# Kernel tuning notes

Measured on AMD Instinct MI355X. Metric: run time of the kernel, lower is better.

## Reference

```python
import jax, jax.numpy as jnp
import numpy as np

EPS = 1e-5  # torch BatchNorm2d default eps


def _lin(x, W, b):
    # torch nn.Linear: y = x @ W.T + b, W is [out, in]
    return jnp.einsum('...i,oi->...o', x, W) + b


def _bn(x, g, b):
    # BatchNorm2d in training mode: normalize per channel (last axis here)
    # over all other axes (B, N, K) with biased variance.
    m = jnp.mean(x, axis=(0, 1, 2), keepdims=True)
    v = jnp.mean(jnp.square(x - m), axis=(0, 1, 2), keepdims=True)
    return (x - m) * jax.lax.rsqrt(v + EPS) * g + b


def _gelu(x):
    return jax.nn.gelu(x, approximate=False)  # torch F.gelu default is erf


def _knn_idx(points, k):
    # squared euclidean pairwise distances, then k smallest per query
    pn = jnp.sum(points * points, axis=-1)  # [B,N]
    d2 = pn[:, :, None] + pn[:, None, :] - 2.0 * jnp.einsum('bnd,bmd->bnm', points, points)
    _, idx = jax.lax.top_k(-d2, k)  # [B,N,k], nearest first (includes self)
    return idx


def _gather(x, idx):
    # x: [B,N,D], idx: [B,N,K] -> [B,N,K,D]
    return jax.vmap(lambda a, i: a[i])(x, idx)


def setup_inputs() -> dict:
    key = jax.random.key(0)
    ks = jax.random.split(key, 20)
    B, N, Dp, Df, k = 2, 8192, 3, 128, 16

    def lin_params(kw, kb, din, dout):
        s = 1.0 / np.sqrt(din)
        W = jax.random.uniform(kw, (dout, din), jnp.float32, -s, s)
        b = jax.random.uniform(kb, (dout,), jnp.float32, -s, s)
        return W, b

    Wq, bq = lin_params(ks[0], ks[1], Df, Df)
    Wk, bk = lin_params(ks[2], ks[3], Df, Df)
    Wv, bv = lin_params(ks[4], ks[5], Df, Df)
    Wd1, bd1 = lin_params(ks[6], ks[7], Dp, Dp)
    Wd2, bd2 = lin_params(ks[8], ks[9], Dp, Df)
    Wg1, bg1 = lin_params(ks[10], ks[11], Df, Df)
    Wg2, bg2 = lin_params(ks[12], ks[13], Df, Df)

    return {
        'feats': jax.random.normal(ks[14], (B, N, Df), jnp.float32),
        'points': jax.random.normal(ks[15], (B, N, Dp), jnp.float32),
        'Wq': Wq, 'bq': bq, 'Wk': Wk, 'bk': bk, 'Wv': Wv, 'bv': bv,
        'Wd1': Wd1, 'bd1': bd1, 'Wd2': Wd2, 'bd2': bd2,
        'Wg1': Wg1, 'bg1': bg1, 'Wg2': Wg2, 'bg2': bg2,
        'gd': jnp.ones((Dp,), jnp.float32), 'betad': jnp.zeros((Dp,), jnp.float32),
        'gg1': jnp.ones((Df,), jnp.float32), 'betag1': jnp.zeros((Df,), jnp.float32),
        'gg2': jnp.ones((Df,), jnp.float32), 'betag2': jnp.zeros((Df,), jnp.float32),
        'k': 16,
    }


def reference(feats, points, Wq, bq, Wk, bk, Wv, bv, Wd1, bd1, Wd2, bd2,
              Wg1, bg1, Wg2, bg2, gd, betad, gg1, betag1, gg2, betag2, k):
    idx = _knn_idx(points, k)                     # [B,N,k]
    knn_feats = _gather(feats, idx)               # [B,N,k,Df]
    knn_points = _gather(points, idx)             # [B,N,k,Dp]

    pos = points[:, :, None, :] - knn_points      # [B,N,k,Dp]
    pos = _lin(pos, Wd1, bd1)
    pos = _gelu(_bn(pos, gd, betad))
    pos = _lin(pos, Wd2, bd2)                     # [B,N,k,Df]

    q = _lin(feats, Wq, bq)                       # [B,N,Df]
    key_t = _lin(knn_feats, Wk, bk)               # [B,N,k,Df]
    gamma = q[:, :, None, :] - key_t + pos
    gamma = _gelu(_bn(gamma, gg1, betag1))
    gamma = _lin(gamma, Wg1, bg1)
    gamma = _gelu(_bn(gamma, gg2, betag2))
    gamma = _lin(gamma, Wg2, bg2)

    rho = jax.nn.softmax(gamma, axis=-2)          # softmax over k neighbors
    value = _lin(knn_feats, Wv, bv) + pos
    return jnp.einsum('bnkd,bnkd->bnd', rho, value)
```

## Files before the change

kernel.cpp:

```cpp
#include <hip/hip_runtime.h>
#include <hip/hip_bf16.h>
#include <math.h>

#define NPTS 8192
#define STAT_CNT 262144.0f
#define BN_EPS 1e-5f

typedef __attribute__((__ext_vector_type__(8))) __bf16 bf16x8;
typedef __attribute__((__ext_vector_type__(4))) float f32x4;

#define SD_SUM 0
#define SD_SSQ 4
#define SD_SC 8
#define SD_SH 12
#define SG1_SC 16
#define SG1_SH 144
#define SG2_SC 272
#define SG2_SH 400
#define PG1 528
#define PG2 8720
#define STATS_FLOATS 16912

__device__ __forceinline__ unsigned short f2b(float x){
  unsigned u = __float_as_uint(x);
  return (unsigned short)((u + 0x7FFFu + ((u>>16)&1u)) >> 16);
}
__device__ __forceinline__ float b2f(unsigned short h){
  return __uint_as_float(((unsigned)h)<<16);
}
__device__ __forceinline__ float gelu_f(float x){
  float u = fabsf(x)*0.70710678118654752440f;
  float t = 1.0f/fmaf(0.3275911f, u, 1.0f);
  float p = t*fmaf(t,fmaf(t,fmaf(t,fmaf(t,1.061405429f,-1.453152027f),1.421413741f),-0.284496736f),0.254829592f);
  float er = fmaf(-p, __expf(-u*u), 1.0f);
  er = (x < 0.f) ? -er : er;
  return 0.5f*x*(1.0f+er);
}
__device__ __forceinline__ int swz(int row, int byteInRow){
  return row*256 + (byteInRow ^ ((row&7)<<4));
}
__device__ __forceinline__ float dist2f(float qx,float qy,float qz,float qpn,
                                        float x,float y,float z,float w){
  return (qpn + w) - 2.0f*fmaf(qx,x,fmaf(qy,y,qz*z));
}

#define MFMA16(a,b,c) __builtin_amdgcn_mfma_f32_16x16x32_bf16((a),(b),(c),0,0,0)

__device__ __forceinline__ bf16x8 ldsA8(const unsigned short* sA, int row, int k){
  return *(const bf16x8*)((const char*)sA + swz(row, k*2));
}
__device__ __forceinline__ bf16x8 ldW8(const unsigned short* W, int n, int k){
  return *(const bf16x8*)(W + n*128 + k);
}

__global__ __launch_bounds__(256) void k_prep(
    const float* __restrict__ feats, const float* __restrict__ Wq, const float* __restrict__ Wk,
    const float* __restrict__ Wv, const float* __restrict__ Wg1, const float* __restrict__ Wg2,
    unsigned short* __restrict__ wbf, unsigned short* __restrict__ featb, float* __restrict__ stats)
{
  int i = blockIdx.x*256 + threadIdx.x;
  featb[i] = f2b(feats[i]);
  if (i < 16384){
    wbf[i]        = f2b(Wq[i]);
    wbf[16384+i]  = f2b(Wk[i]);
    wbf[32768+i]  = f2b(Wv[i]);
    wbf[49152+i]  = f2b(Wg1[i]);
    wbf[65536+i]  = f2b(Wg2[i]);
  }
  if (i < STATS_FLOATS) stats[i] = 0.f;
}

__global__ __launch_bounds__(256) void k_knn5(const float* __restrict__ points, int* __restrict__ idxb){
  __shared__ float svD[16][64];
  __shared__ int   svI[16][64];
  __shared__ int   svC[16];
  int tid = threadIdx.x;
  int wid = tid>>6, lane = tid&63;
  int blk = blockIdx.x;
  int b = (blk*16) >> 13;
  const float* cb = points + (size_t)b*NPTS*3;
  int qbase = blk*16 + wid*4;
  float qx[4],qy[4],qz[4],qpn[4],lmin[4],tq[4];
  #pragma unroll
  for (int q=0;q<4;++q){
    const float* qp = points + (size_t)(qbase+q)*3;
    qx[q]=qp[0]; qy[q]=qp[1]; qz[q]=qp[2];
    qpn[q]=fmaf(qz[q],qz[q],fmaf(qy[q],qy[q],qx[q]*qx[q]));
    lmin[q]=3.4e38f;
  }
  if (lane < 4) svC[wid*4+lane] = 0;
  #pragma unroll 4
  for (int s=0;s<128;++s){
    int p = s*64 + lane;
    const float* sp = cb + (size_t)p*3;
    float x=sp[0], y=sp[1], z=sp[2];
    float w = fmaf(z,z,fmaf(y,y,x*x));
    #pragma unroll
    for (int q=0;q<4;++q){
      float d = dist2f(qx[q],qy[q],qz[q],qpn[q], x,y,z,w);
      lmin[q] = fminf(lmin[q], d);
    }
  }
  #pragma unroll
  for (int q=0;q<4;++q){
    float v = lmin[q];
    #pragma unroll
    for (int k=2;k<=64;k<<=1){
      #pragma unroll
      for (int j=k>>1;j>=1;j>>=1){
        float o = __shfl_xor(v, j);
        bool keepmin = ((lane & j)==0) == ((lane & k)==0);
        v = keepmin ? fminf(v,o) : fmaxf(v,o);
      }
    }
    tq[q] = __shfl(v, 15);
  }
  #pragma unroll 2
  for (int s=0;s<128;++s){
    int p = s*64 + lane;
    const float* sp = cb + (size_t)p*3;
    float x=sp[0], y=sp[1], z=sp[2];
    float w = fmaf(z,z,fmaf(y,y,x*x));
    #pragma unroll
    for (int q=0;q<4;++q){
      float d = dist2f(qx[q],qy[q],qz[q],qpn[q], x,y,z,w);
      if (d <= tq[q]){
        int wq = wid*4+q;
        int slot = atomicAdd(&svC[wq], 1);
        if (slot < 64){ svD[wq][slot]=d; svI[wq][slot]=p; }
      }
    }
  }
  __syncthreads();
  #pragma unroll 1
  for (int q=0;q<4;++q){
    int wq = wid*4+q;
    int n = svC[wq]; n = (n>64)?64:n;
    float d = (lane<n)? svD[wq][lane] : 3.4e38f;
    int   ii = (lane<n)? svI[wq][lane] : 0x7fffffff;
    int rank = 0;
    #pragma unroll 4
    for (int j=0;j<n;++j){
      float od = svD[wq][j]; int oi = svI[wq][j];
      rank += ((od<d)||(od==d && oi<ii)) ? 1 : 0;
    }
    if (lane<n && rank<16) idxb[(size_t)(qbase+q)*16 + rank] = ii;
  }
}

__global__ __launch_bounds__(256) void k_dstats(const int* __restrict__ idxb,
    const float* __restrict__ points, const float* __restrict__ Wd1, const float* __restrict__ bd1,
    float* __restrict__ stats){
  __shared__ float sS[6];
  if (threadIdx.x < 6) sS[threadIdx.x]=0.f;
  __syncthreads();
  int qi = blockIdx.x*256 + threadIdx.x;
  int b = qi >> 13;
  const float* qp = points + (size_t)qi*3;
  float qx=qp[0],qy=qp[1],qz=qp[2];
  float w00=Wd1[0],w01=Wd1[1],w02=Wd1[2],w10=Wd1[3],w11=Wd1[4],w12=Wd1[5],w20=Wd1[6],w21=Wd1[7],w22=Wd1[8];
  float b0=bd1[0],b1=bd1[1],b2=bd1[2];
  float s0=0,s1=0,s2=0,q0=0,q1=0,q2=0;
  #pragma unroll
  for (int j=0;j<16;j++){
    int nb = idxb[(size_t)qi*16 + j];
    const float* np_ = points + (size_t)(b*NPTS + nb)*3;
    float dx=qx-np_[0], dy=qy-np_[1], dz=qz-np_[2];
    float t0 = fmaf(dz,w02,fmaf(dy,w01,dx*w00)) + b0;
    float t1 = fmaf(dz,w12,fmaf(dy,w11,dx*w10)) + b1;
    float t2 = fmaf(dz,w22,fmaf(dy,w21,dx*w20)) + b2;
    s0+=t0; s1+=t1; s2+=t2;
    q0=fmaf(t0,t0,q0); q1=fmaf(t1,t1,q1); q2=fmaf(t2,t2,q2);
  }
  atomicAdd(&sS[0],s0); atomicAdd(&sS[1],s1); atomicAdd(&sS[2],s2);
  atomicAdd(&sS[3],q0); atomicAdd(&sS[4],q1); atomicAdd(&sS[5],q2);
  __syncthreads();
  if (threadIdx.x < 3) atomicAdd(&stats[SD_SUM+threadIdx.x], sS[threadIdx.x]);
  else if (threadIdx.x < 6) atomicAdd(&stats[SD_SSQ+threadIdx.x-3], sS[threadIdx.x]);
}

__global__ void k_finalize(float* stats, int sumOff, int ssqOff, const float* __restrict__ gm,
                           const float* __restrict__ bt, int scOff, int shOff, int C){
  int c = blockIdx.x*64 + threadIdx.x;
  if (c >= C) return;
  float m = stats[sumOff+c] * (1.0f/STAT_CNT);
  float v = stats[ssqOff+c] * (1.0f/STAT_CNT) - m*m;
  v = fmaxf(v, 0.0f);
  float rs = rsqrtf(v + BN_EPS);
  float sc = gm[c]*rs;
  stats[scOff+c] = sc;
  stats[shOff+c] = fmaf(-m, sc, bt[c]);
}

__global__ void k_finalizeP(float* stats, int partOff, const float* __restrict__ gm,
                            const float* __restrict__ bt, int scOff, int shOff){
  int c = blockIdx.x*64 + threadIdx.x;
  float s=0.f, q=0.f;
  #pragma unroll 4
  for (int p=0;p<32;p++){
    s += stats[partOff + p*256 + c];
    q += stats[partOff + p*256 + 128 + c];
  }
  float m = s * (1.0f/STAT_CNT);
  float v = fmaxf(q*(1.0f/STAT_CNT) - m*m, 0.0f);
  float rs = rsqrtf(v + BN_EPS);
  float sc = gm[c]*rs;
  stats[scOff+c] = sc;
  stats[shOff+c] = fmaf(-m, sc, bt[c]);
}

__global__ __launch_bounds__(256) void k_qkv(
    const unsigned short* __restrict__ featb, const unsigned short* __restrict__ wbf,
    const float* __restrict__ bq, const float* __restrict__ bk, const float* __restrict__ bv,
    float* __restrict__ qout, unsigned short* __restrict__ kout, unsigned short* __restrict__ vout)
{
  __shared__ __align__(16) unsigned short sA[64*128];
  int tid = threadIdx.x;
  size_t row0g = (size_t)blockIdx.x*64;
  for (int t=tid; t<1024; t+=256){
    int row=t>>4, cc=t&15;
    uint4 v = *(const uint4*)(featb + (row0g+row)*128 + cc*8);
    *(uint4*)((char*)sA + swz(row, cc*16)) = v;
  }
  __syncthreads();
  int wid=tid>>6, lane=tid&63;
  int r=lane&15, g=lane>>4;
  int row0 = wid*16;
  f32x4 aQ[8]={}, aK[8]={}, aV[8]={};
  const unsigned short* WQ = wbf;
  const unsigned short* WK = wbf+16384;
  const unsigned short* WV = wbf+32768;
  #pragma unroll
  for (int ks=0;ks<4;++ks){
    int k = ks*32 + g*8;
    bf16x8 a0 = ldsA8(sA, row0+r, k);
    #pragma unroll
    for (int nt=0;nt<8;++nt){
      aQ[nt]=MFMA16(a0, ldW8(WQ,nt*16+r,k), aQ[nt]);
      aK[nt]=MFMA16(a0, ldW8(WK,nt*16+r,k), aK[nt]);
      aV[nt]=MFMA16(a0, ldW8(WV,nt*16+r,k), aV[nt]);
    }
  }
  #pragma unroll
  for (int nt=0;nt<8;++nt){
    int ch=nt*16+r;
    float bqc=bq[ch], bkc=bk[ch], bvc=bv[ch];
    #pragma unroll
    for (int rr=0;rr<4;++rr){
      size_t grow = row0g + row0 + g*4 + rr;
      qout[grow*128+ch] = aQ[nt][rr]+bqc;
      kout[grow*128+ch] = f2b(aK[nt][rr]+bkc);
      vout[grow*128+ch] = f2b(aV[nt][rr]+bvc);
    }
  }
}

__global__ __launch_bounds__(256) void k_fuse(
    const float* __restrict__ points, const int* __restrict__ idxb,
    const float* __restrict__ qbuf, const unsigned short* __restrict__ kb,
    const unsigned short* __restrict__ vb,
    const float* __restrict__ Wd1, const float* __restrict__ bd1,
    const float* __restrict__ Wd2, const float* __restrict__ bd2,
    float* __restrict__ stats,
    unsigned short* __restrict__ g1out, unsigned short* __restrict__ valout)
{
  __shared__ float sSum[128];
  __shared__ float sSq[128];
  int tid = threadIdx.x, blk = blockIdx.x;
  int slot = tid & 15, jg = tid >> 4;
  int lane = tid & 63;
  int ch0 = slot*8;
  if (tid < 128){ sSum[tid]=0.f; sSq[tid]=0.f; }
  float w2[24], b2v[8];
  #pragma unroll
  for (int u=0;u<8;++u){
    w2[u*3+0]=Wd2[(ch0+u)*3+0];
    w2[u*3+1]=Wd2[(ch0+u)*3+1];
    w2[u*3+2]=Wd2[(ch0+u)*3+2];
    b2v[u]=bd2[ch0+u];
  }
  int c = slot & 3; c = (c==3)?2:c;
  float wa  = (c==0)?Wd1[0]:((c==1)?Wd1[3]:Wd1[6]);
  float wb_ = (c==0)?Wd1[1]:((c==1)?Wd1[4]:Wd1[7]);
  float wc  = (c==0)?Wd1[2]:((c==1)?Wd1[5]:Wd1[8]);
  float bc_ = (c==0)?bd1[0]:((c==1)?bd1[1]:bd1[2]);
  float sc_ = (c==0)?stats[SD_SC+0]:((c==1)?stats[SD_SC+1]:stats[SD_SC+2]);
  float sh_ = (c==0)?stats[SD_SH+0]:((c==1)?stats[SD_SH+1]:stats[SD_SH+2]);
  int base = lane & 48;
  float accS[8]={0,0,0,0,0,0,0,0}, accQ[8]={0,0,0,0,0,0,0,0};
  __syncthreads();
  #pragma unroll 2
  for (int i=0;i<8;++i){
    int q = blk*8 + i;
    int b = q >> 13;
    int row = q*16 + jg;
    int nb = idxb[row];
    const float* ctr = points + (size_t)q*3;
    const float* np_ = points + (size_t)(b*NPTS + nb)*3;
    float dx = ctr[0]-np_[0], dy = ctr[1]-np_[1], dz = ctr[2]-np_[2];
    float t = fmaf(dz, wc, fmaf(dy, wb_, dx*wa)) + bc_;
    float tc = gelu_f(fmaf(t, sc_, sh_));
    float g0  = __shfl(tc, base+0);
    float g1v = __shfl(tc, base+1);
    float g2v = __shfl(tc, base+2);
    size_t kvoff = ((size_t)(b*NPTS + nb))*128 + ch0;
    union { uint4 u; unsigned short s[8]; } K, V, G, Vo;
    K.u = *(const uint4*)(kb + kvoff);
    V.u = *(const uint4*)(vb + kvoff);
    float4 q0 = *(const float4*)(qbuf + (size_t)q*128 + ch0);
    float4 q1 = *(const float4*)(qbuf + (size_t)q*128 + ch0 + 4);
    float qv[8] = {q0.x,q0.y,q0.z,q0.w,q1.x,q1.y,q1.z,q1.w};
    #pragma unroll
    for (int u=0;u<8;++u){
      float pos = fmaf(g2v, w2[u*3+2], fmaf(g1v, w2[u*3+1], g0*w2[u*3+0])) + b2v[u];
      float key = b2f(K.s[u]);
      float val = b2f(V.s[u]) + pos;
      float gmv = qv[u] - key + pos;
      accS[u] += gmv; accQ[u] = fmaf(gmv,gmv,accQ[u]);
      G.s[u] = f2b(gmv); Vo.s[u] = f2b(val);
    }
    *(uint4*)(g1out + (size_t)row*128 + ch0) = G.u;
    *(uint4*)(valout + (size_t)row*128 + ch0) = Vo.u;
  }
  #pragma unroll
  for (int u=0;u<8;++u){
    atomicAdd(&sSum[ch0+u], accS[u]);
    atomicAdd(&sSq[ch0+u], accQ[u]);
  }
  __syncthreads();
  if (tid < 128){
    int ps = blk & 31;
    atomicAdd(&stats[PG1 + ps*256 + tid], sSum[tid]);
    atomicAdd(&stats[PG1 + ps*256 + 128 + tid], sSq[tid]);
  }
}

__global__ __launch_bounds__(256) void k_g(
    const unsigned short* __restrict__ gin, const unsigned short* __restrict__ W,
    const float* __restrict__ bias, float* __restrict__ stats, int scOff, int shOff,
    unsigned short* __restrict__ gout, int partOff)
{
  __shared__ __align__(16) unsigned short sA[64*128];
  __shared__ float sSum[128];
  __shared__ float sSq[128];
  int tid = threadIdx.x;
  size_t row0 = (size_t)blockIdx.x*64;
  if (tid<128){ sSum[tid]=0.f; sSq[tid]=0.f; }
  for (int t=tid; t<1024; t+=256){
    int row=t>>4, c=t&15;
    union { uint4 u; unsigned short s[8]; } iv, ov;
    iv.u = *(const uint4*)(gin + (row0+row)*128 + c*8);
    #pragma unroll
    for (int u=0;u<8;u++){
      int ch = c*8+u;
      float x = b2f(iv.s[u]);
      x = gelu_f(fmaf(x, stats[scOff+ch], stats[shOff+ch]));
      ov.s[u] = f2b(x);
    }
    *(uint4*)((char*)sA + swz(row, c*16)) = ov.u;
  }
  __syncthreads();
  int wid=tid>>6, lane=tid&63;
  int r=lane&15, g=lane>>4;
  int row0l = wid*16;
  f32x4 acc[8] = {};
  #pragma unroll
  for (int ks=0;ks<4;++ks){
    int k = ks*32 + g*8;
    bf16x8 a0 = ldsA8(sA, row0l+r, k);
    #pragma unroll
    for (int nt=0;nt<8;++nt)
      acc[nt] = MFMA16(a0, ldW8(W,nt*16+r,k), acc[nt]);
  }
  #pragma unroll
  for (int nt=0;nt<8;++nt){
    int ch = nt*16+r;
    float bc = bias[ch];
    float s_=0.f, qq=0.f;
    #pragma unroll
    for (int rr=0;rr<4;++rr){
      int row = row0l + g*4 + rr;
      float x = acc[nt][rr] + bc;
      s_ += x; qq = fmaf(x,x,qq);
      gout[(row0+row)*128 + ch] = f2b(x);
    }
    atomicAdd(&sSum[ch], s_); atomicAdd(&sSq[ch], qq);
  }
  __syncthreads();
  if (tid<128){
    int slot = blockIdx.x & 31;
    atomicAdd(&stats[partOff + slot*256 + tid], sSum[tid]);
    atomicAdd(&stats[partOff + slot*256 + 128 + tid], sSq[tid]);
  }
}

__global__ __launch_bounds__(256) void k_out(
    const unsigned short* __restrict__ gin, const unsigned short* __restrict__ W,
    const float* __restrict__ bias, const float* __restrict__ stats, int scOff, int shOff,
    const unsigned short* __restrict__ val, float* __restrict__ outp)
{
  __shared__ __align__(16) unsigned short sA[64*128];
  __shared__ __align__(16) unsigned short sV[64*128];
  int tid=threadIdx.x;
  size_t row0=(size_t)blockIdx.x*64;
  for (int t=tid;t<1024;t+=256){
    int row=t>>4,c=t&15;
    union { uint4 u; unsigned short s[8]; } iv, ov;
    iv.u = *(const uint4*)(gin + (row0+row)*128 + c*8);
    #pragma unroll
    for (int u=0;u<8;u++){
      int ch=c*8+u;
      float x = b2f(iv.s[u]);
      x = gelu_f(fmaf(x, stats[scOff+ch], stats[shOff+ch]));
      ov.s[u]=f2b(x);
    }
    *(uint4*)((char*)sA + swz(row,c*16)) = ov.u;
    uint4 vv = *(const uint4*)(val + (row0+row)*128 + c*8);
    *(uint4*)((char*)sV + swz(row,c*16)) = vv;
  }
  __syncthreads();
  int wid=tid>>6, lane=tid&63;
  int r=lane&15, g=lane>>4;
  int row0l = wid*16;
  f32x4 acc[8] = {};
  #pragma unroll
  for (int ks=0;ks<4;++ks){
    int k = ks*32 + g*8;
    bf16x8 a0 = ldsA8(sA, row0l+r, k);
    #pragma unroll
    for (int nt=0;nt<8;++nt)
      acc[nt] = MFMA16(a0, ldW8(W,nt*16+r,k), acc[nt]);
  }
  #pragma unroll
  for (int nt=0;nt<8;++nt){
    int ch=nt*16+r; float bc=bias[ch];
    float g3[4], vv[4];
    #pragma unroll
    for (int rr=0;rr<4;++rr){
      int row=row0l+g*4+rr;
      g3[rr]=acc[nt][rr]+bc;
      vv[rr]=b2f(*(const unsigned short*)((const char*)sV + swz(row, ch*2)));
    }
    float m = fmaxf(fmaxf(g3[0],g3[1]),fmaxf(g3[2],g3[3]));
    m = fmaxf(m, __shfl_xor(m,16));
    m = fmaxf(m, __shfl_xor(m,32));
    float s=0.f, o=0.f;
    #pragma unroll
    for (int rr=0;rr<4;++rr){
      float e = __expf(g3[rr]-m);
      s += e; o = fmaf(e, vv[rr], o);
    }
    s += __shfl_xor(s,16); s += __shfl_xor(s,32);
    o += __shfl_xor(o,16); o += __shfl_xor(o,32);
    if (g==0){
      outp[((size_t)blockIdx.x*4 + wid)*128 + ch] = o/s;
    }
  }
}

extern "C" void kernel_launch(void* const* d_in, const int* in_sizes, int n_in,
                              void* d_out, int out_size, void* d_ws, size_t ws_size,
                              hipStream_t stream)
{
  const float* feats  = (const float*)d_in[0];
  const float* points = (const float*)d_in[1];
  const float* Wq = (const float*)d_in[2];  const float* bq = (const float*)d_in[3];
  const float* Wk = (const float*)d_in[4];  const float* bk = (const float*)d_in[5];
  const float* Wv = (const float*)d_in[6];  const float* bv = (const float*)d_in[7];
  const float* Wd1= (const float*)d_in[8];  const float* bd1= (const float*)d_in[9];
  const float* Wd2= (const float*)d_in[10]; const float* bd2= (const float*)d_in[11];
  const float* Wg1= (const float*)d_in[12]; const float* bg1= (const float*)d_in[13];
  const float* Wg2= (const float*)d_in[14]; const float* bg2= (const float*)d_in[15];
  const float* gd = (const float*)d_in[16]; const float* betad = (const float*)d_in[17];
  const float* gg1= (const float*)d_in[18]; const float* betag1= (const float*)d_in[19];
  const float* gg2= (const float*)d_in[20]; const float* betag2= (const float*)d_in[21];
  float* outp = (float*)d_out;

  char* ws = (char*)d_ws;
  int*    idxb  = (int*)   (ws + 0);
  float*  stats = (float*) (ws + 1048576);
  unsigned short* wbf   = (unsigned short*)(ws + 1179648);
  unsigned short* featb = (unsigned short*)(ws + 1343488);
  unsigned short* kb    = (unsigned short*)(ws + 5537792);
  unsigned short* vbuf  = (unsigned short*)(ws + 9732096);
  unsigned short* g1b = (unsigned short*)(ws + 13926400);
  unsigned short* vab = (unsigned short*)(ws + 81035264);
  unsigned short* g2b = (unsigned short*)(ws + 148144128);
  float*  qbuf  = (float*) (ws + 215252992);

  k_prep<<<dim3(8192),dim3(256),0,stream>>>(feats,Wq,Wk,Wv,Wg1,Wg2,wbf,featb,stats);
  k_knn5<<<dim3(1024),dim3(256),0,stream>>>(points,idxb);
  k_dstats<<<dim3(64),dim3(256),0,stream>>>(idxb,points,Wd1,bd1,stats);
  k_finalize<<<dim3(1),dim3(64),0,stream>>>(stats,SD_SUM,SD_SSQ,gd,betad,SD_SC,SD_SH,3);
  k_qkv<<<dim3(256),dim3(256),0,stream>>>(featb,wbf,bq,bk,bv,qbuf,kb,vbuf);
  k_fuse<<<dim3(2048),dim3(256),0,stream>>>(points,idxb,qbuf,kb,vbuf,Wd1,bd1,Wd2,bd2,stats,g1b,vab);
  k_finalizeP<<<dim3(2),dim3(64),0,stream>>>(stats,PG1,gg1,betag1,SG1_SC,SG1_SH);
  k_g<<<dim3(4096),dim3(256),0,stream>>>(g1b,wbf+49152,bg1,stats,SG1_SC,SG1_SH,g2b,PG2);
  k_finalizeP<<<dim3(2),dim3(64),0,stream>>>(stats,PG2,gg2,betag2,SG2_SC,SG2_SH);
  k_out<<<dim3(4096),dim3(256),0,stream>>>(g2b,wbf+65536,bg2,stats,SG2_SC,SG2_SH,vab,outp);
  (void)in_sizes; (void)n_in; (void)out_size; (void)ws_size;
}
```

Before: 409.8 us.

## Stage weights in LDS, load A directly to registers, persistent grid in k_g/k_out

k_g and k_out become persistent kernels: 1024 blocks of 512 threads, each wave looping over two 16-row tiles. The 128x128 bf16 weight matrix is staged once per block in swizzled LDS instead of being re-read from global per MFMA, and the BN scale/shift is cached in LDS. A fragments are loaded straight from global and run through a vectorised BN+GELU+bf16 pack into registers, skipping the LDS staging of activations. Stats are reduced per wave in registers and shuffles before the global atomics, replacing the per-block LDS atomics. The risks are uncoalesced direct A loads and value reads, and fewer waves in flight to hide memory latency.

```diff
diff --git a/kernel.cpp b/kernel.cpp
--- a/kernel.cpp
+++ b/kernel.cpp
@@ -51,6 +51,24 @@
 }
 __device__ __forceinline__ bf16x8 ldW8(const unsigned short* W, int n, int k){
   return *(const bf16x8*)(W + n*128 + k);
+}
+
+__device__ __forceinline__ bf16x8 bn_gelu8(uint4 raw, const float* sSC, const float* sSH, int kb0){
+  union { f32x4 v[2]; float f[8]; } SC, SH;
+  SC.v[0] = *(const f32x4*)&sSC[kb0]; SC.v[1] = *(const f32x4*)&sSC[kb0+4];
+  SH.v[0] = *(const f32x4*)&sSH[kb0]; SH.v[1] = *(const f32x4*)&sSH[kb0+4];
+  union { uint4 u; unsigned int w[4]; } U; U.u = raw;
+  union { unsigned int w[4]; bf16x8 v; } O;
+  #pragma unroll
+  for (int p=0;p<4;++p){
+    float xlo = gelu_f(fmaf(__uint_as_float(U.w[p]<<16),        SC.f[2*p],   SH.f[2*p]));
+    float xhi = gelu_f(fmaf(__uint_as_float(U.w[p]&0xffff0000u), SC.f[2*p+1], SH.f[2*p+1]));
+    unsigned lo = __float_as_uint(xlo), hi = __float_as_uint(xhi);
+    lo = (lo + 0x7FFFu + ((lo>>16)&1u)) >> 16;
+    hi = (hi + 0x7FFFu + ((hi>>16)&1u)) & 0xffff0000u;
+    O.w[p] = hi | lo;
+  }
+  return O.v;
 }
 
 __global__ __launch_bounds__(256) void k_prep(
@@ -335,125 +353,122 @@
   }
 }
 
-__global__ __launch_bounds__(256) void k_g(
+__global__ __launch_bounds__(512) void k_g(
     const unsigned short* __restrict__ gin, const unsigned short* __restrict__ W,
     const float* __restrict__ bias, float* __restrict__ stats, int scOff, int shOff,
     unsigned short* __restrict__ gout, int partOff)
 {
-  __shared__ __align__(16) unsigned short sA[64*128];
-  __shared__ float sSum[128];
-  __shared__ float sSq[128];
+  __shared__ __align__(16) unsigned short sW[128*128];
+  __shared__ float sSC[128], sSH[128];
   int tid = threadIdx.x;
-  size_t row0 = (size_t)blockIdx.x*64;
-  if (tid<128){ sSum[tid]=0.f; sSq[tid]=0.f; }
-  for (int t=tid; t<1024; t+=256){
+  for (int t=tid; t<2048; t+=512){
     int row=t>>4, c=t&15;
-    union { uint4 u; unsigned short s[8]; } iv, ov;
-    iv.u = *(const uint4*)(gin + (row0+row)*128 + c*8);
-    #pragma unroll
-    for (int u=0;u<8;u++){
-      int ch = c*8+u;
-      float x = b2f(iv.s[u]);
-      x = gelu_f(fmaf(x, stats[scOff+ch], stats[shOff+ch]));
-      ov.s[u] = f2b(x);
-    }
-    *(uint4*)((char*)sA + swz(row, c*16)) = ov.u;
-  }
+    uint4 v = *(const uint4*)(W + row*128 + c*8);
+    *(uint4*)((char*)sW + swz(row,c*16)) = v;
+  }
+  if (tid < 128){ sSC[tid]=stats[scOff+tid]; sSH[tid]=stats[shOff+tid]; }
   __syncthreads();
   int wid=tid>>6, lane=tid&63;
   int r=lane&15, g=lane>>4;
-  int row0l = wid*16;
-  f32x4 acc[8] = {};
-  #pragma unroll
-  for (int ks=0;ks<4;++ks){
-    int k = ks*32 + g*8;
-    bf16x8 a0 = ldsA8(sA, row0l+r, k);
-    #pragma unroll
-    for (int nt=0;nt<8;++nt)
-      acc[nt] = MFMA16(a0, ldW8(W,nt*16+r,k), acc[nt]);
+  float bs[8];
+  #pragma unroll
+  for (int nt=0;nt<8;++nt) bs[nt]=bias[nt*16+r];
+  float accS[8]={0,0,0,0,0,0,0,0}, accQ[8]={0,0,0,0,0,0,0,0};
+  for (int tile = blockIdx.x*8 + wid; tile < 16384; tile += 8192){
+    size_t row0 = (size_t)tile*16;
+    bf16x8 a[4];
+    #pragma unroll
+    for (int ks=0;ks<4;++ks){
+      int kb0 = ks*32 + g*8;
+      uint4 raw = *(const uint4*)(gin + (row0+r)*128 + kb0);
+      a[ks] = bn_gelu8(raw, sSC, sSH, kb0);
+    }
+    f32x4 acc[8] = {};
+    #pragma unroll
+    for (int ks=0;ks<4;++ks){
+      int k = ks*32 + g*8;
+      #pragma unroll
+      for (int nt=0;nt<8;++nt)
+        acc[nt] = MFMA16(a[ks], ldsA8(sW, nt*16+r, k), acc[nt]);
+    }
+    #pragma unroll
+    for (int nt=0;nt<8;++nt){
+      #pragma unroll
+      for (int rr=0;rr<4;++rr){
+        float x = acc[nt][rr] + bs[nt];
+        accS[nt] += x; accQ[nt] = fmaf(x,x,accQ[nt]);
+        gout[(row0 + g*4 + rr)*128 + nt*16 + r] = f2b(x);
+      }
+    }
   }
   #pragma unroll
   for (int nt=0;nt<8;++nt){
-    int ch = nt*16+r;
-    float bc = bias[ch];
-    float s_=0.f, qq=0.f;
-    #pragma unroll
-    for (int rr=0;rr<4;++rr){
-      int row = row0l + g*4 + rr;
-      float x = acc[nt][rr] + bc;
-      s_ += x; qq = fmaf(x,x,qq);
-      gout[(row0+row)*128 + ch] = f2b(x);
-    }
-    atomicAdd(&sSum[ch], s_); atomicAdd(&sSq[ch], qq);
-  }
-  __syncthreads();
-  if (tid<128){
-    int slot = blockIdx.x & 31;
-    atomicAdd(&stats[partOff + slot*256 + tid], sSum[tid]);
-    atomicAdd(&stats[partOff + slot*256 + 128 + tid], sSq[tid]);
-  }
-}
-
-__global__ __launch_bounds__(256) void k_out(
+    float s_ = accS[nt], q_ = accQ[nt];
+    s_ += __shfl_xor(s_,16); s_ += __shfl_xor(s_,32);
+    q_ += __shfl_xor(q_,16); q_ += __shfl_xor(q_,32);
+    if (g==0){
+      int slot = blockIdx.x & 31;
+      atomicAdd(&stats[partOff + slot*256 + nt*16+r], s_);
+      atomicAdd(&stats[partOff + slot*256 + 128 + nt*16+r], q_);
+    }
+  }
+}
+
+__global__ __launch_bounds__(512) void k_out(
     const unsigned short* __restrict__ gin, const unsigned short* __restrict__ W,
     const float* __restrict__ bias, const float* __restrict__ stats, int scOff, int shOff,
     const unsigned short* __restrict__ val, float* __restrict__ outp)
 {
-  __shared__ __align__(16) unsigned short sA[64*128];
-  __shared__ __align__(16) unsigned short sV[64*128];
-  int tid=threadIdx.x;
-  size_t row0=(size_t)blockIdx.x*64;
-  for (int t=tid;t<1024;t+=256){
-    int row=t>>4,c=t&15;
-    union { uint4 u; unsigned short s[8]; } iv, ov;
-    iv.u = *(const uint4*)(gin + (row0+row)*128 + c*8);
-    #pragma unroll
-    for (int u=0;u<8;u++){
-      int ch=c*8+u;
-      float x = b2f(iv.s[u]);
-      x = gelu_f(fmaf(x, stats[scOff+ch], stats[shOff+ch]));
-      ov.s[u]=f2b(x);
-    }
-    *(uint4*)((char*)sA + swz(row,c*16)) = ov.u;
-    uint4 vv = *(const uint4*)(val + (row0+row)*128 + c*8);
-    *(uint4*)((char*)sV + swz(row,c*16)) = vv;
-  }
+  __shared__ __align__(16) unsigned short sW[128*128];
+  __shared__ float sSC[128], sSH[128];
+  int tid = threadIdx.x;
+  for (int t=tid; t<2048; t+=512){
+    int row=t>>4, c=t&15;
+    uint4 v = *(const uint4*)(W + row*128 + c*8);
+    *(uint4*)((char*)sW + swz(row,c*16)) = v;
+  }
+  if (tid < 128){ sSC[tid]=stats[scOff+tid]; sSH[tid]=stats[shOff+tid]; }
   __syncthreads();
   int wid=tid>>6, lane=tid&63;
   int r=lane&15, g=lane>>4;
-  int row0l = wid*16;
-  f32x4 acc[8] = {};
-  #pragma unroll
-  for (int ks=0;ks<4;++ks){
-    int k = ks*32 + g*8;
-    bf16x8 a0 = ldsA8(sA, row0l+r, k);
-    #pragma unroll
-    for (int nt=0;nt<8;++nt)
-      acc[nt] = MFMA16(a0, ldW8(W,nt*16+r,k), acc[nt]);
-  }
-  #pragma unroll
-  for (int nt=0;nt<8;++nt){
-    int ch=nt*16+r; float bc=bias[ch];
-    float g3[4], vv[4];
-    #pragma unroll
-    for (int rr=0;rr<4;++rr){
-      int row=row0l+g*4+rr;
-      g3[rr]=acc[nt][rr]+bc;
-      vv[rr]=b2f(*(const unsigned short*)((const char*)sV + swz(row, ch*2)));
-    }
-    float m = fmaxf(fmaxf(g3[0],g3[1]),fmaxf(g3[2],g3[3]));
-    m = fmaxf(m, __shfl_xor(m,16));
-    m = fmaxf(m, __shfl_xor(m,32));
-    float s=0.f, o=0.f;
-    #pragma unroll
-    for (int rr=0;rr<4;++rr){
-      float e = __expf(g3[rr]-m);
-      s += e; o = fmaf(e, vv[rr], o);
-    }
-    s += __shfl_xor(s,16); s += __shfl_xor(s,32);
-    o += __shfl_xor(o,16); o += __shfl_xor(o,32);
-    if (g==0){
-      outp[((size_t)blockIdx.x*4 + wid)*128 + ch] = o/s;
+  float bs[8];
+  #pragma unroll
+  for (int nt=0;nt<8;++nt) bs[nt]=bias[nt*16+r];
+  for (int tile = blockIdx.x*8 + wid; tile < 16384; tile += 8192){
+    size_t row0 = (size_t)tile*16;
+    bf16x8 a[4];
+    #pragma unroll
+    for (int ks=0;ks<4;++ks){
+      int kb0 = ks*32 + g*8;
+      uint4 raw = *(const uint4*)(gin + (row0+r)*128 + kb0);
+      a[ks] = bn_gelu8(raw, sSC, sSH, kb0);
+    }
+    f32x4 acc[8] = {};
+    #pragma unroll
+    for (int ks=0;ks<4;++ks){
+      int k = ks*32 + g*8;
+      #pragma unroll
+      for (int nt=0;nt<8;++nt)
+        acc[nt] = MFMA16(a[ks], ldsA8(sW, nt*16+r, k), acc[nt]);
+    }
+    #pragma unroll
+    for (int nt=0;nt<8;++nt){
+      float g3[4];
+      #pragma unroll
+      for (int rr=0;rr<4;++rr) g3[rr] = acc[nt][rr] + bs[nt];
+      float m = fmaxf(fmaxf(g3[0],g3[1]),fmaxf(g3[2],g3[3]));
+      m = fmaxf(m, __shfl_xor(m,16));
+      m = fmaxf(m, __shfl_xor(m,32));
+      float s=0.f, o=0.f;
+      #pragma unroll
+      for (int rr=0;rr<4;++rr){
+        float e = __expf(g3[rr]-m);
+        float vv = b2f(val[(row0 + g*4 + rr)*128 + nt*16 + r]);
+        s += e; o = fmaf(e, vv, o);
+      }
+      s += __shfl_xor(s,16); s += __shfl_xor(s,32);
+      o += __shfl_xor(o,16); o += __shfl_xor(o,32);
+      if (g==0) outp[(size_t)tile*128 + nt*16 + r] = o/s;
     }
   }
 }
@@ -495,8 +510,8 @@
   k_qkv<<<dim3(256),dim3(256),0,stream>>>(featb,wbf,bq,bk,bv,qbuf,kb,vbuf);
   k_fuse<<<dim3(2048),dim3(256),0,stream>>>(points,idxb,qbuf,kb,vbuf,Wd1,bd1,Wd2,bd2,stats,g1b,vab);
   k_finalizeP<<<dim3(2),dim3(64),0,stream>>>(stats,PG1,gg1,betag1,SG1_SC,SG1_SH);
-  k_g<<<dim3(4096),dim3(256),0,stream>>>(g1b,wbf+49152,bg1,stats,SG1_SC,SG1_SH,g2b,PG2);
+  k_g<<<dim3(1024),dim3(512),0,stream>>>(g1b,wbf+49152,bg1,stats,SG1_SC,SG1_SH,g2b,PG2);
   k_finalizeP<<<dim3(2),dim3(64),0,stream>>>(stats,PG2,gg2,betag2,SG2_SC,SG2_SH);
-  k_out<<<dim3(4096),dim3(256),0,stream>>>(g2b,wbf+65536,bg2,stats,SG2_SC,SG2_SH,vab,outp);
+  k_out<<<dim3(1024),dim3(512),0,stream>>>(g2b,wbf+65536,bg2,stats,SG2_SC,SG2_SH,vab,outp);
   (void)in_sizes; (void)n_in; (void)out_size; (void)ws_size;
 }
```

New measurement: 348.5 us, median of 2. 1.18x faster.
